# Performance work log

Measured on AMD Instinct MI355X. Metric: run time of the kernel, lower is better.

Reference implementation:

```python
import jax, jax.numpy as jnp
import numpy as np

IN_C, H1, H2, FC1, NCLS = 16, 32, 64, 128, 10
N_NODES, N_EDGES = 20000, 100000


def _glorot(key, shape):
    fan_in, fan_out = shape[0], shape[-1]
    s = jnp.sqrt(6.0 / (fan_in + fan_out))
    return jax.random.uniform(key, shape, jnp.float32, -s, s)


def setup_inputs() -> dict:
    key = jax.random.key(0)
    ks = jax.random.split(key, 20)
    x = jax.random.normal(ks[0], (N_NODES, IN_C), jnp.float32)
    edge_index = jax.random.randint(ks[1], (2, N_EDGES), 0, N_NODES, jnp.int64)
    edge_attr = jax.random.uniform(ks[2], (N_EDGES, 1), jnp.float32)
    return {
        "x": x,
        "edge_index": edge_index,
        "edge_attr": edge_attr,
        # conv1 edge-MLP: 1 -> 25 -> IN_C*H1
        "w1a": _glorot(ks[3], (1, 25)), "b1a": jnp.zeros((25,), jnp.float32),
        "w1b": _glorot(ks[4], (25, IN_C * H1)), "b1b": jnp.zeros((IN_C * H1,), jnp.float32),
        "wr1": _glorot(ks[5], (IN_C, H1)), "bias1": jnp.zeros((H1,), jnp.float32),
        # conv2 edge-MLP: 1 -> 25 -> H1*H2 (=2048)
        "w2a": _glorot(ks[6], (1, 25)), "b2a": jnp.zeros((25,), jnp.float32),
        "w2b": _glorot(ks[7], (25, H1 * H2)), "b2b": jnp.zeros((H1 * H2,), jnp.float32),
        "wr2": _glorot(ks[8], (H1, H2)), "bias2": jnp.zeros((H2,), jnp.float32),
        # trailing FCs
        "fc1_w": _glorot(ks[9], (H2, FC1)), "fc1_b": jnp.zeros((FC1,), jnp.float32),
        "fc2_w": _glorot(ks[10], (FC1, NCLS)), "fc2_b": jnp.zeros((NCLS,), jnp.float32),
    }


def _nnconv(x, src, tgt, edge_attr, wa, ba, wb, bb, wroot, bias, in_c, out_c):
    # per-edge MLP-generated weight matrix [E, in_c, out_c]
    h = jax.nn.relu(edge_attr @ wa + ba) @ wb + bb
    W = h.reshape(-1, in_c, out_c)
    # gather source feats, per-edge matmul, scatter-max to targets
    msg = jnp.einsum("ei,eio->eo", x[src], W)  # [E, out_c]
    agg = jax.ops.segment_max(msg, tgt, num_segments=x.shape[0])
    agg = jnp.where(jnp.isfinite(agg), agg, 0.0)  # nodes with no in-edges -> 0 (PyG behavior)
    return agg + x @ wroot + bias


def reference(x, edge_index, edge_attr,
              w1a, b1a, w1b, b1b, wr1, bias1,
              w2a, b2a, w2b, b2b, wr2, bias2,
              fc1_w, fc1_b, fc2_w, fc2_b):
    src, tgt = edge_index[0], edge_index[1]
    h = jax.nn.elu(_nnconv(x, src, tgt, edge_attr, w1a, b1a, w1b, b1b, wr1, bias1, IN_C, H1))
    h = jax.nn.elu(_nnconv(h, src, tgt, edge_attr, w2a, b2a, w2b, b2b, wr2, bias2, H1, H2))
    h = jax.nn.elu(h @ fc1_w + fc1_b)
    h = h @ fc2_w + fc2_b
    return jax.nn.log_softmax(h, axis=1)
```

## Files before the change

kernel.cpp:

```cpp
#include <hip/hip_runtime.h>
#include <float.h>
#include <math.h>


#define NCONST 25
#define CH1 32
#define CH2 16
#define PACK_MASK 0x1FFFF
#define TNB 4

__device__ __forceinline__ void atomicMaxFloat(float* addr, float val) {
    if (val >= 0.f) atomicMax((int*)addr, __float_as_int(val));
    else            atomicMin((unsigned int*)addr, __float_as_uint(val));
}
__device__ __forceinline__ float readlane_f(float v, int l) {
    return __int_as_float(__builtin_amdgcn_readlane(__float_as_int(v), l));
}
__device__ __forceinline__ float elu_f(float a) {
    return a > 0.f ? a : expm1f(a);
}

__global__ void fill_kernel(float* agg, int nAgg, int* ords, int nOrd, int* hist, int nH) {
    int i = blockIdx.x * blockDim.x + threadIdx.x;
    int stride = gridDim.x * blockDim.x;
    int total = nAgg + nOrd + nH;
    for (; i < total; i += stride) {
        if (i < nAgg) agg[i] = -FLT_MAX;
        else if (i < nAgg + nOrd) ords[i - nAgg] = -1;
        else hist[i - nAgg - nOrd] = 0;
    }
}

__global__ void assign_hist_kernel(const float* __restrict__ ea,
                                   const float* __restrict__ w1a, const float* __restrict__ b1a,
                                   const float* __restrict__ w2a, const float* __restrict__ b2a,
                                   int E, int* __restrict__ segpack, int* __restrict__ hist) {
    __shared__ float t1[NCONST], t2[NCONST];
    __shared__ int lh[64];
    int tid = threadIdx.x;
    if (tid < NCONST) {
        float w = w1a[tid]; t1[tid] = (w != 0.f) ? (-b1a[tid] / w) : INFINITY;
        float v = w2a[tid]; t2[tid] = (v != 0.f) ? (-b2a[tid] / v) : INFINITY;
    }
    if (tid < 64) lh[tid] = 0;
    __syncthreads();
    int e = blockIdx.x * blockDim.x + tid;
    bool valid = e < E;
    if (valid) {
        float a = ea[e];
        int j1 = 0, j2 = 0;
        for (int k = 0; k < NCONST; ++k) { j1 += (t1[k] < a); j2 += (t2[k] < a); }
        segpack[e] = j1 | (j2 << 8);
        atomicAdd(&lh[j1], 1); atomicAdd(&lh[32 + j2], 1);
    }
    __syncthreads();
    if (tid < 64 && lh[tid]) atomicAdd(&hist[tid], lh[tid]);
}

__global__ void scanpad_kernel(const int* __restrict__ hist, int* __restrict__ cur) {
    __shared__ int h[64];
    int tid = threadIdx.x;
    h[tid] = hist[tid];
    __syncthreads();
    if (tid == 0) {
        int off = 0;
        for (int j = 0; j < 26; ++j) { cur[j] = off; off += ((h[j] + CH1 - 1) / CH1) * CH1; }
    } else if (tid == 1) {
        int off = 0;
        for (int j = 0; j < 26; ++j) { cur[32 + j] = off; off += ((h[32 + j] + CH2 - 1) / CH2) * CH2; }
    }
}

__global__ void scatter_kernel(const int* __restrict__ segpack, int E, int* __restrict__ cur,
                               int* __restrict__ order1, int* __restrict__ order2) {
    __shared__ int lh[64], lb[64];
    int tid = threadIdx.x;
    if (tid < 64) lh[tid] = 0;
    __syncthreads();
    int e = blockIdx.x * blockDim.x + tid;
    bool valid = e < E;
    int j1 = 0, j2 = 0, r1 = 0, r2 = 0;
    if (valid) {
        int p = segpack[e]; j1 = p & 0xFF; j2 = p >> 8;
        r1 = atomicAdd(&lh[j1], 1); r2 = atomicAdd(&lh[32 + j2], 1);
    }
    __syncthreads();
    if (tid < 64 && lh[tid]) lb[tid] = atomicAdd(&cur[tid], lh[tid]);
    __syncthreads();
    if (valid) {
        order1[lb[j1] + r1] = (j1 << 17) | e;
        order2[lb[32 + j2] + r2] = (j2 << 17) | e;
    }
}

__global__ void build_uv_fused(const float* w1a, const float* b1a, const float* w1b, const float* b1b,
                               const float* w2a, const float* b2a, const float* w2b, const float* b2b,
                               float* U1, float* V1, float* U2, float* V2) {
    __shared__ float swa[NCONST], sba[NCONST], st[NCONST];
    __shared__ int sr[NCONST];
    __shared__ unsigned msk_sh;
    int seg = blockIdx.y;
    int bx = blockIdx.x;
    int conv = (bx < 2) ? 0 : 1;
    const float* wa = conv ? w2a : w1a;
    const float* ba = conv ? b2a : b1a;
    int tid = threadIdx.x;
    if (tid < NCONST) {
        float w = wa[tid], b = ba[tid];
        swa[tid] = w; sba[tid] = b;
        st[tid] = (w != 0.f) ? (-b / w) : INFINITY;
    }
    __syncthreads();
    if (tid < NCONST) {
        int rk = 0;
        for (int l = 0; l < NCONST; ++l) rk += (st[l] < st[tid]) ? 1 : 0;
        sr[tid] = rk;
    }
    __syncthreads();
    if (tid == 0) {
        unsigned m = 0;
        for (int k = 0; k < NCONST; ++k) {
            float w = swa[k];
            bool act = (w > 0.f) ? (seg > sr[k])
                     : (w < 0.f) ? (seg <= sr[k])
                                 : (sba[k] > 0.f);
            if (act) m |= (1u << k);
        }
        msk_sh = m;
    }
    __syncthreads();
    unsigned msk = msk_sh;
    if (conv == 0) {
        int idx = bx * 256 + tid;
        float u = 0.f, v = 0.f;
        for (int k = 0; k < NCONST; ++k)
            if (msk & (1u << k)) { float w = w1b[k * 512 + idx]; u = fmaf(swa[k], w, u); v = fmaf(sba[k], w, v); }
        v += b1b[idx];
        U1[seg * 512 + idx] = u; V1[seg * 512 + idx] = v;
    } else {
        int idx = (bx - 2) * 256 + tid;
        float u = 0.f, v = 0.f;
        for (int k = 0; k < NCONST; ++k)
            if (msk & (1u << k)) { float w = w2b[k * 2048 + idx]; u = fmaf(swa[k], w, u); v = fmaf(sba[k], w, v); }
        v += b2b[idx];
        U2[seg * 2048 + idx] = u; V2[seg * 2048 + idx] = v;
    }
}

__global__ void edge1_kernel(const float* __restrict__ xin, const int* __restrict__ src,
                             const int* __restrict__ tgt, const float* __restrict__ ea,
                             const int* __restrict__ order, int cap,
                             const float* __restrict__ U, const float* __restrict__ V,
                             float* __restrict__ agg) {
    int wid = (blockIdx.x * blockDim.x + threadIdx.x) >> 6;
    int lane = threadIdx.x & 63;
    int base = wid * CH1;
    if (base >= cap) return;
    int pk = order[base + (lane & (CH1 - 1))];
    int p0 = __builtin_amdgcn_readfirstlane(pk);
    if (p0 < 0) return;
    int seg = p0 >> 17;
    int ev = (pk < 0) ? 0 : (pk & PACK_MASK);
    int sv = src[ev], tv = tgt[ev];
    float av = ea[ev];
    int half = lane >> 5, c = lane & 31;
    float Ur[16], Vr[16];
    {
        const float* Us = U + seg * 512 + c;
        const float* Vs = V + seg * 512 + c;
#pragma unroll
        for (int i = 0; i < 16; ++i) { Ur[i] = Us[i * 32]; Vr[i] = Vs[i * 32]; }
    }
#pragma unroll
    for (int t = 0; t < CH1; t += 2) {
        int pA = __builtin_amdgcn_readlane(pk, t);
        int pB = __builtin_amdgcn_readlane(pk, t + 1);
        int sA = __builtin_amdgcn_readlane(sv, t);
        int sB = __builtin_amdgcn_readlane(sv, t + 1);
        int tA = __builtin_amdgcn_readlane(tv, t);
        int tB = __builtin_amdgcn_readlane(tv, t + 1);
        float aA = readlane_f(av, t);
        float aB = readlane_f(av, t + 1);
        const float* xA = xin + sA * 16;
        const float* xB = xin + sB * 16;
        float ah = half ? aB : aA;
        int   th = half ? tB : tA;
        int   ph = half ? pB : pA;
        float acc = 0.f;
#pragma unroll
        for (int i = 0; i < 16; ++i) {
            float xi = half ? xB[i] : xA[i];
            acc = fmaf(xi, fmaf(ah, Ur[i], Vr[i]), acc);
        }
        if (ph >= 0) atomicMaxFloat(&agg[th * 32 + c], acc);
    }
}

__global__ void edge2_kernel(const float* __restrict__ xin, const int* __restrict__ src,
                             const int* __restrict__ tgt, const float* __restrict__ ea,
                             const int* __restrict__ order, int cap,
                             const float* __restrict__ U, const float* __restrict__ V,
                             float* __restrict__ agg) {
    int wid = (blockIdx.x * blockDim.x + threadIdx.x) >> 6;
    int lane = threadIdx.x & 63;
    int base = wid * CH2;
    if (base >= cap) return;
    int pk = order[base + (lane & (CH2 - 1))];
    int p0 = __builtin_amdgcn_readfirstlane(pk);
    if (p0 < 0) return;
    int seg = p0 >> 17;
    int ev = (pk < 0) ? 0 : (pk & PACK_MASK);
    int sv = src[ev], tv = tgt[ev];
    float av = ea[ev];
    float Ur[32], Vr[32];
    {
        const float* Us = U + seg * 2048 + lane;
        const float* Vs = V + seg * 2048 + lane;
#pragma unroll
        for (int i = 0; i < 32; ++i) { Ur[i] = Us[i * 64]; Vr[i] = Vs[i * 64]; }
    }
#pragma unroll
    for (int t = 0; t < CH2; t += 2) {
        int pA = __builtin_amdgcn_readlane(pk, t);
        int pB = __builtin_amdgcn_readlane(pk, t + 1);
        int sA = __builtin_amdgcn_readlane(sv, t);
        int sB = __builtin_amdgcn_readlane(sv, t + 1);
        int tA = __builtin_amdgcn_readlane(tv, t);
        int tB = __builtin_amdgcn_readlane(tv, t + 1);
        float aA = readlane_f(av, t);
        float aB = readlane_f(av, t + 1);
        const float* xA = xin + sA * 32;
        const float* xB = xin + sB * 32;
        float accA = 0.f, accB = 0.f;
#pragma unroll
        for (int i = 0; i < 32; ++i) {
            accA = fmaf(xA[i], fmaf(aA, Ur[i], Vr[i]), accA);
            accB = fmaf(xB[i], fmaf(aB, Ur[i], Vr[i]), accB);
        }
        if (pA >= 0) atomicMaxFloat(&agg[tA * 64 + lane], accA);
        if (pB >= 0) atomicMaxFloat(&agg[tB * 64 + lane], accB);
    }
}

__global__ void node1_kernel(const float* __restrict__ xin, const float* __restrict__ agg,
                             const float* __restrict__ wroot, const float* __restrict__ bias,
                             float* __restrict__ out, int N) {
    int idx = blockIdx.x * blockDim.x + threadIdx.x;
    if (idx >= N * 32) return;
    int n = idx >> 5, c = idx & 31;
    float v = agg[idx];
    if (v == -FLT_MAX) v = 0.f;
    float acc = v + bias[c];
#pragma unroll
    for (int i = 0; i < 16; ++i) acc = fmaf(xin[n * 16 + i], wroot[i * 32 + c], acc);
    out[idx] = acc > 0.f ? acc : expm1f(acc);
}

__global__ void tail_kernel(const float* __restrict__ h1, const float* __restrict__ agg2,
                            const float* __restrict__ wr2, const float* __restrict__ bias2,
                            const float* __restrict__ fc1w, const float* __restrict__ fc1b,
                            const float* __restrict__ fc2w, const float* __restrict__ fc2b,
                            float* __restrict__ out) {
    __shared__ __align__(16) float h1sh[4][TNB][32];
    __shared__ __align__(16) float h2sh[4][TNB][64];
    __shared__ __align__(16) float h3sh[4][TNB][132];
    __shared__ __align__(16) float wTsh[10][132];
    int tid = threadIdx.x;
    int wv = tid >> 6, lane = tid & 63;

    for (int t = tid; t < 1280; t += 256) {
        int k = t / 10, j = t - k * 10;
        wTsh[j][k] = fc2w[t];
    }
    __syncthreads();

    int nb = blockIdx.x * (4 * TNB) + wv * TNB;

    {
        const float2* hp = (const float2*)(h1 + (size_t)nb * 32);
        ((float2*)&h1sh[wv][0][0])[lane] = hp[lane];
    }

    float b2v = bias2[lane];
    float ac0 = agg2[(size_t)(nb + 0) * 64 + lane];
    float ac1 = agg2[(size_t)(nb + 1) * 64 + lane];
    float ac2 = agg2[(size_t)(nb + 2) * 64 + lane];
    float ac3 = agg2[(size_t)(nb + 3) * 64 + lane];
    ac0 = (ac0 == -FLT_MAX ? 0.f : ac0) + b2v;
    ac1 = (ac1 == -FLT_MAX ? 0.f : ac1) + b2v;
    ac2 = (ac2 == -FLT_MAX ? 0.f : ac2) + b2v;
    ac3 = (ac3 == -FLT_MAX ? 0.f : ac3) + b2v;
#pragma unroll 8
    for (int i = 0; i < 32; ++i) {
        float w = wr2[i * 64 + lane];
        ac0 = fmaf(h1sh[wv][0][i], w, ac0);
        ac1 = fmaf(h1sh[wv][1][i], w, ac1);
        ac2 = fmaf(h1sh[wv][2][i], w, ac2);
        ac3 = fmaf(h1sh[wv][3][i], w, ac3);
    }
    h2sh[wv][0][lane] = elu_f(ac0);
    h2sh[wv][1][lane] = elu_f(ac1);
    h2sh[wv][2][lane] = elu_f(ac2);
    h2sh[wv][3][lane] = elu_f(ac3);

    float fb1 = fc1b[lane], fb2 = fc1b[64 + lane];
    float p0 = fb1, p1 = fb1, p2 = fb1, p3 = fb1;
    float q0 = fb2, q1 = fb2, q2 = fb2, q3 = fb2;
#pragma unroll 2
    for (int k4 = 0; k4 < 16; ++k4) {
        int k = k4 * 4;
        float wA0 = fc1w[(k + 0) * 128 + lane];
        float wB0 = fc1w[(k + 0) * 128 + 64 + lane];
        float wA1 = fc1w[(k + 1) * 128 + lane];
        float wB1 = fc1w[(k + 1) * 128 + 64 + lane];
        float wA2 = fc1w[(k + 2) * 128 + lane];
        float wB2 = fc1w[(k + 2) * 128 + 64 + lane];
        float wA3 = fc1w[(k + 3) * 128 + lane];
        float wB3 = fc1w[(k + 3) * 128 + 64 + lane];
        float4 g0 = ((const float4*)h2sh[wv][0])[k4];
        float4 g1 = ((const float4*)h2sh[wv][1])[k4];
        float4 g2 = ((const float4*)h2sh[wv][2])[k4];
        float4 g3 = ((const float4*)h2sh[wv][3])[k4];
        p0 = fmaf(g0.x, wA0, p0); p0 = fmaf(g0.y, wA1, p0);
        p0 = fmaf(g0.z, wA2, p0); p0 = fmaf(g0.w, wA3, p0);
        q0 = fmaf(g0.x, wB0, q0); q0 = fmaf(g0.y, wB1, q0);
        q0 = fmaf(g0.z, wB2, q0); q0 = fmaf(g0.w, wB3, q0);
        p1 = fmaf(g1.x, wA0, p1); p1 = fmaf(g1.y, wA1, p1);
        p1 = fmaf(g1.z, wA2, p1); p1 = fmaf(g1.w, wA3, p1);
        q1 = fmaf(g1.x, wB0, q1); q1 = fmaf(g1.y, wB1, q1);
        q1 = fmaf(g1.z, wB2, q1); q1 = fmaf(g1.w, wB3, q1);
        p2 = fmaf(g2.x, wA0, p2); p2 = fmaf(g2.y, wA1, p2);
        p2 = fmaf(g2.z, wA2, p2); p2 = fmaf(g2.w, wA3, p2);
        q2 = fmaf(g2.x, wB0, q2); q2 = fmaf(g2.y, wB1, q2);
        q2 = fmaf(g2.z, wB2, q2); q2 = fmaf(g2.w, wB3, q2);
        p3 = fmaf(g3.x, wA0, p3); p3 = fmaf(g3.y, wA1, p3);
        p3 = fmaf(g3.z, wA2, p3); p3 = fmaf(g3.w, wA3, p3);
        q3 = fmaf(g3.x, wB0, q3); q3 = fmaf(g3.y, wB1, q3);
        q3 = fmaf(g3.z, wB2, q3); q3 = fmaf(g3.w, wB3, q3);
    }
    h3sh[wv][0][lane] = elu_f(p0); h3sh[wv][0][64 + lane] = elu_f(q0);
    h3sh[wv][1][lane] = elu_f(p1); h3sh[wv][1][64 + lane] = elu_f(q1);
    h3sh[wv][2][lane] = elu_f(p2); h3sh[wv][2][64 + lane] = elu_f(q2);
    h3sh[wv][3][lane] = elu_f(p3); h3sh[wv][3][64 + lane] = elu_f(q3);

    {
        int n = lane >> 4, j = lane & 15;
        bool act = j < 10;
        int jc = act ? j : 0;
        float a = fc2b[jc];
        const float4* h3v = (const float4*)h3sh[wv][n];
        const float4* wv4 = (const float4*)wTsh[jc];
#pragma unroll
        for (int q = 0; q < 32; ++q) {
            float4 h = h3v[q];
            float4 w = wv4[q];
            a = fmaf(h.x, w.x, a);
            a = fmaf(h.y, w.y, a);
            a = fmaf(h.z, w.z, a);
            a = fmaf(h.w, w.w, a);
        }
        float lm = act ? a : -FLT_MAX;
        lm = fmaxf(lm, __shfl_xor(lm, 1, 16));
        lm = fmaxf(lm, __shfl_xor(lm, 2, 16));
        lm = fmaxf(lm, __shfl_xor(lm, 4, 16));
        lm = fmaxf(lm, __shfl_xor(lm, 8, 16));
        float ls = act ? expf(a - lm) : 0.f;
        ls += __shfl_xor(ls, 1, 16);
        ls += __shfl_xor(ls, 2, 16);
        ls += __shfl_xor(ls, 4, 16);
        ls += __shfl_xor(ls, 8, 16);
        if (act) out[(size_t)(nb + n) * 10 + j] = a - lm - logf(ls);
    }
}

extern "C" void kernel_launch(void* const* d_in, const int* in_sizes, int n_in,
                              void* d_out, int out_size, void* d_ws, size_t ws_size,
                              hipStream_t stream) {
    const float* x     = (const float*)d_in[0];
    const int*   eidx  = (const int*)d_in[1];
    const float* ea    = (const float*)d_in[2];
    const float* w1a   = (const float*)d_in[3];
    const float* b1a   = (const float*)d_in[4];
    const float* w1b   = (const float*)d_in[5];
    const float* b1b   = (const float*)d_in[6];
    const float* wr1   = (const float*)d_in[7];
    const float* bias1 = (const float*)d_in[8];
    const float* w2a   = (const float*)d_in[9];
    const float* b2a   = (const float*)d_in[10];
    const float* w2b   = (const float*)d_in[11];
    const float* b2b   = (const float*)d_in[12];
    const float* wr2   = (const float*)d_in[13];
    const float* bias2 = (const float*)d_in[14];
    const float* fc1w  = (const float*)d_in[15];
    const float* fc1b  = (const float*)d_in[16];
    const float* fc2w  = (const float*)d_in[17];
    const float* fc2b  = (const float*)d_in[18];

    const int N = in_sizes[0] / 16;
    const int E = in_sizes[2];
    const int* src = eidx;
    const int* tgt = eidx + E;

    const int cap1 = ((E + 26 * (CH1 - 1)) + CH1 - 1) / CH1 * CH1;
    const int cap2 = ((E + 26 * (CH2 - 1)) + CH2 - 1) / CH2 * CH2;

    float* ws = (float*)d_ws;
    size_t off = 0;
    int*      hist = (int*)(ws + off);      off += 64;
    int*      cur  = (int*)(ws + off);      off += 64;
    int*      segp = (int*)(ws + off);      off += E;
    int*      ord1 = (int*)(ws + off);      off += cap1;
    int*      ord2 = (int*)(ws + off);      off += cap2;
    float*    U1   = ws + off;              off += 26 * 512;
    float*    V1   = ws + off;              off += 26 * 512;
    float*    U2   = ws + off;              off += 26 * 2048;
    float*    V2   = ws + off;              off += 26 * 2048;
    float*    AGG1 = ws + off;              off += (size_t)N * 32;
    float*    AGG2 = ws + off;              off += (size_t)N * 64;
    float*    H1b  = ws + off;              off += (size_t)N * 32;

    fill_kernel<<<512, 256, 0, stream>>>(AGG1, N * 96, ord1, cap1 + cap2, hist, 64);
    assign_hist_kernel<<<(E + 255) / 256, 256, 0, stream>>>(ea, w1a, b1a, w2a, b2a, E, segp, hist);
    scanpad_kernel<<<1, 64, 0, stream>>>(hist, cur);
    scatter_kernel<<<(E + 255) / 256, 256, 0, stream>>>(segp, E, cur, ord1, ord2);
    build_uv_fused<<<dim3(10, 26), 256, 0, stream>>>(w1a, b1a, w1b, b1b, w2a, b2a, w2b, b2b,
                                                     U1, V1, U2, V2);
    {
        int waves = cap1 / CH1;
        edge1_kernel<<<(waves + 3) / 4, 256, 0, stream>>>(x, src, tgt, ea, ord1, cap1, U1, V1, AGG1);
    }
    node1_kernel<<<(N * 32 + 255) / 256, 256, 0, stream>>>(x, AGG1, wr1, bias1, H1b, N);
    {
        int waves = cap2 / CH2;
        edge2_kernel<<<(waves + 3) / 4, 256, 0, stream>>>(H1b, src, tgt, ea, ord2, cap2, U2, V2, AGG2);
    }
    tail_kernel<<<N / 16, 256, 0, stream>>>(H1b, AGG2, wr2, bias2, fc1w, fc1b, fc2w, fc2b, (float*)d_out);
}
```

Before: 198.2 us.

## Fuse whole pipeline into one cooperative persistent kernel with grid syncs

Replaces the nine separate kernel launches with one persistent cooperative kernel. The former kernels become phases separated by grid-wide barriers, and the grid is sized from occupancy up to 512 blocks. The aim is to remove per-launch overhead and inter-kernel gaps. In exchange, phases like edge processing and the tail run with far fewer blocks in grid-stride loops, and grid.sync adds its own cost. The old multi-kernel path remains as a fallback if the cooperative launch fails.

After: 703.4 us. 3.55x slower.

```diff
diff --git a/kernel.cpp b/kernel.cpp
--- a/kernel.cpp
+++ b/kernel.cpp
@@ -1,13 +1,17 @@
 #include <hip/hip_runtime.h>
+#include <hip/hip_cooperative_groups.h>
 #include <float.h>
 #include <math.h>
+
+namespace cg = cooperative_groups;
 
 
 #define NCONST 25
 #define CH1 32
 #define CH2 16
 #define PACK_MASK 0x1FFFF
-#define TNB 4
+#define NBLK_MAX 512
+#define NTHR 256
 
 __device__ __forceinline__ void atomicMaxFloat(float* addr, float val) {
     if (val >= 0.f) atomicMax((int*)addr, __float_as_int(val));
@@ -19,6 +23,366 @@
 __device__ __forceinline__ float elu_f(float a) {
     return a > 0.f ? a : expm1f(a);
 }
+
+struct MegaParams {
+    const float *x; const int *src; const int *tgt; const float *ea;
+    const float *w1a, *b1a, *w1b, *b1b, *wr1, *bias1;
+    const float *w2a, *b2a, *w2b, *b2b, *wr2, *bias2;
+    const float *fc1w, *fc1b, *fc2w, *fc2b;
+    float *out;
+    int *hist, *cur, *segp, *ord1, *ord2;
+    float *U1, *V1, *U2, *V2, *AGG1, *AGG2, *H1b;
+    int N, E, cap1, cap2;
+};
+
+__device__ __forceinline__ void gsync(cg::grid_group& grid) {
+    __threadfence();
+    grid.sync();
+    __threadfence();
+}
+
+__global__ void __launch_bounds__(NTHR) mega_kernel(MegaParams p) {
+    cg::grid_group grid = cg::this_grid();
+
+    __shared__ float t1[NCONST], t2[NCONST];
+    __shared__ int lh[64], lb[64];
+    __shared__ float swa[NCONST], sba[NCONST], stt[NCONST];
+    __shared__ int srk[NCONST];
+    __shared__ unsigned msk_sh;
+    __shared__ __align__(16) float h1sh[4][4][32];
+    __shared__ __align__(16) float h2sh[4][4][64];
+    __shared__ __align__(16) float h3sh[4][4][132];
+    __shared__ __align__(16) float wTsh[10][132];
+
+    const int tid  = threadIdx.x;
+    const int gtid = blockIdx.x * NTHR + tid;
+    const int gsz  = gridDim.x * NTHR;
+    const int lane = tid & 63;
+    const int wv   = tid >> 6;
+
+    {
+        int nAgg = p.N * 96, nOrd = p.cap1 + p.cap2;
+        int total = nAgg + nOrd + 64;
+        for (int i = gtid; i < total; i += gsz) {
+            if (i < nAgg) p.AGG1[i] = -FLT_MAX;
+            else if (i < nAgg + nOrd) p.ord1[i - nAgg] = -1;
+            else p.hist[i - nAgg - nOrd] = 0;
+        }
+        for (int v = blockIdx.x; v < 260; v += gridDim.x) {
+            int seg = v / 10;
+            int bx  = v % 10;
+            int conv = (bx < 2) ? 0 : 1;
+            const float* wa = conv ? p.w2a : p.w1a;
+            const float* ba = conv ? p.b2a : p.b1a;
+            if (tid < NCONST) {
+                float w = wa[tid], b = ba[tid];
+                swa[tid] = w; sba[tid] = b;
+                stt[tid] = (w != 0.f) ? (-b / w) : INFINITY;
+            }
+            __syncthreads();
+            if (tid < NCONST) {
+                int rk = 0;
+                for (int l = 0; l < NCONST; ++l) rk += (stt[l] < stt[tid]) ? 1 : 0;
+                srk[tid] = rk;
+            }
+            __syncthreads();
+            if (tid == 0) {
+                unsigned m = 0;
+                for (int k = 0; k < NCONST; ++k) {
+                    float w = swa[k];
+                    bool act = (w > 0.f) ? (seg > srk[k])
+                             : (w < 0.f) ? (seg <= srk[k])
+                                         : (sba[k] > 0.f);
+                    if (act) m |= (1u << k);
+                }
+                msk_sh = m;
+            }
+            __syncthreads();
+            unsigned msk = msk_sh;
+            if (conv == 0) {
+                int idx = bx * 256 + tid;
+                float u = 0.f, vv = 0.f;
+                for (int k = 0; k < NCONST; ++k)
+                    if (msk & (1u << k)) { float w = p.w1b[k * 512 + idx]; u = fmaf(swa[k], w, u); vv = fmaf(sba[k], w, vv); }
+                vv += p.b1b[idx];
+                p.U1[seg * 512 + idx] = u; p.V1[seg * 512 + idx] = vv;
+            } else {
+                int idx = (bx - 2) * 256 + tid;
+                float u = 0.f, vv = 0.f;
+                for (int k = 0; k < NCONST; ++k)
+                    if (msk & (1u << k)) { float w = p.w2b[k * 2048 + idx]; u = fmaf(swa[k], w, u); vv = fmaf(sba[k], w, vv); }
+                vv += p.b2b[idx];
+                p.U2[seg * 2048 + idx] = u; p.V2[seg * 2048 + idx] = vv;
+            }
+            __syncthreads();
+        }
+    }
+    gsync(grid);
+
+    {
+        if (tid < NCONST) {
+            float w = p.w1a[tid]; t1[tid] = (w != 0.f) ? (-p.b1a[tid] / w) : INFINITY;
+            float v2 = p.w2a[tid]; t2[tid] = (v2 != 0.f) ? (-p.b2a[tid] / v2) : INFINITY;
+        }
+        __syncthreads();
+        for (int base = blockIdx.x * NTHR; base < p.E; base += gsz) {
+            if (tid < 64) lh[tid] = 0;
+            __syncthreads();
+            int e = base + tid;
+            if (e < p.E) {
+                float a = p.ea[e];
+                int j1 = 0, j2 = 0;
+                for (int k = 0; k < NCONST; ++k) { j1 += (t1[k] < a); j2 += (t2[k] < a); }
+                p.segp[e] = j1 | (j2 << 8);
+                atomicAdd(&lh[j1], 1); atomicAdd(&lh[32 + j2], 1);
+            }
+            __syncthreads();
+            if (tid < 64 && lh[tid]) atomicAdd(&p.hist[tid], lh[tid]);
+            __syncthreads();
+        }
+    }
+    gsync(grid);
+
+    if (blockIdx.x == 0) {
+        if (tid == 0) {
+            int off = 0;
+            for (int j = 0; j < 26; ++j) { p.cur[j] = off; off += ((p.hist[j] + CH1 - 1) / CH1) * CH1; }
+        } else if (tid == 1) {
+            int off = 0;
+            for (int j = 0; j < 26; ++j) { p.cur[32 + j] = off; off += ((p.hist[32 + j] + CH2 - 1) / CH2) * CH2; }
+        }
+    }
+    gsync(grid);
+
+    {
+        for (int base = blockIdx.x * NTHR; base < p.E; base += gsz) {
+            if (tid < 64) lh[tid] = 0;
+            __syncthreads();
+            int e = base + tid;
+            bool valid = e < p.E;
+            int j1 = 0, j2 = 0, r1 = 0, r2 = 0;
+            if (valid) {
+                int pk = p.segp[e]; j1 = pk & 0xFF; j2 = pk >> 8;
+                r1 = atomicAdd(&lh[j1], 1); r2 = atomicAdd(&lh[32 + j2], 1);
+            }
+            __syncthreads();
+            if (tid < 64 && lh[tid]) lb[tid] = atomicAdd(&p.cur[tid], lh[tid]);
+            __syncthreads();
+            if (valid) {
+                p.ord1[lb[j1] + r1] = (j1 << 17) | e;
+                p.ord2[lb[32 + j2] + r2] = (j2 << 17) | e;
+            }
+            __syncthreads();
+        }
+    }
+    gsync(grid);
+
+    {
+        int gw = gtid >> 6, nw = gsz >> 6;
+        for (int w = gw; w * CH1 < p.cap1; w += nw) {
+            int base = w * CH1;
+            int pk = p.ord1[base + (lane & (CH1 - 1))];
+            int p0 = __builtin_amdgcn_readfirstlane(pk);
+            if (p0 < 0) continue;
+            int seg = p0 >> 17;
+            int ev = (pk < 0) ? 0 : (pk & PACK_MASK);
+            int sv = p.src[ev], tv = p.tgt[ev];
+            float av = p.ea[ev];
+            int half = lane >> 5, c = lane & 31;
+            float Ur[16], Vr[16];
+            {
+                const float* Us = p.U1 + seg * 512 + c;
+                const float* Vs = p.V1 + seg * 512 + c;
+#pragma unroll
+                for (int i = 0; i < 16; ++i) { Ur[i] = Us[i * 32]; Vr[i] = Vs[i * 32]; }
+            }
+#pragma unroll
+            for (int t = 0; t < CH1; t += 2) {
+                int pA = __builtin_amdgcn_readlane(pk, t);
+                int pB = __builtin_amdgcn_readlane(pk, t + 1);
+                int sA = __builtin_amdgcn_readlane(sv, t);
+                int sB = __builtin_amdgcn_readlane(sv, t + 1);
+                int tA = __builtin_amdgcn_readlane(tv, t);
+                int tB = __builtin_amdgcn_readlane(tv, t + 1);
+                float aA = readlane_f(av, t);
+                float aB = readlane_f(av, t + 1);
+                const float* xA = p.x + sA * 16;
+                const float* xB = p.x + sB * 16;
+                float ah = half ? aB : aA;
+                int   th = half ? tB : tA;
+                int   ph = half ? pB : pA;
+                float acc = 0.f;
+#pragma unroll
+                for (int i = 0; i < 16; ++i) {
+                    float xi = half ? xB[i] : xA[i];
+                    acc = fmaf(xi, fmaf(ah, Ur[i], Vr[i]), acc);
+                }
+                if (ph >= 0) atomicMaxFloat(&p.AGG1[th * 32 + c], acc);
+            }
+        }
+    }
+    gsync(grid);
+
+    {
+        for (int idx = gtid; idx < p.N * 32; idx += gsz) {
+            int n = idx >> 5, c = idx & 31;
+            float v = p.AGG1[idx];
+            if (v == -FLT_MAX) v = 0.f;
+            float acc = v + p.bias1[c];
+#pragma unroll
+            for (int i = 0; i < 16; ++i) acc = fmaf(p.x[n * 16 + i], p.wr1[i * 32 + c], acc);
+            p.H1b[idx] = acc > 0.f ? acc : expm1f(acc);
+        }
+    }
+    gsync(grid);
+
+    {
+        int gw = gtid >> 6, nw = gsz >> 6;
+        for (int w = gw; w * CH2 < p.cap2; w += nw) {
+            int base = w * CH2;
+            int pk = p.ord2[base + (lane & (CH2 - 1))];
+            int p0 = __builtin_amdgcn_readfirstlane(pk);
+            if (p0 < 0) continue;
+            int seg = p0 >> 17;
+            int ev = (pk < 0) ? 0 : (pk & PACK_MASK);
+            int sv = p.src[ev], tv = p.tgt[ev];
+            float av = p.ea[ev];
+            float Ur[32], Vr[32];
+            {
+                const float* Us = p.U2 + seg * 2048 + lane;
+                const float* Vs = p.V2 + seg * 2048 + lane;
+#pragma unroll
+                for (int i = 0; i < 32; ++i) { Ur[i] = Us[i * 64]; Vr[i] = Vs[i * 64]; }
+            }
+#pragma unroll
+            for (int t = 0; t < CH2; t += 2) {
+                int pA = __builtin_amdgcn_readlane(pk, t);
+                int pB = __builtin_amdgcn_readlane(pk, t + 1);
+                int sA = __builtin_amdgcn_readlane(sv, t);
+                int sB = __builtin_amdgcn_readlane(sv, t + 1);
+                int tA = __builtin_amdgcn_readlane(tv, t);
+                int tB = __builtin_amdgcn_readlane(tv, t + 1);
+                float aA = readlane_f(av, t);
+                float aB = readlane_f(av, t + 1);
+                const float* xA = p.H1b + sA * 32;
+                const float* xB = p.H1b + sB * 32;
+                float accA = 0.f, accB = 0.f;
+#pragma unroll
+                for (int i = 0; i < 32; ++i) {
+                    accA = fmaf(xA[i], fmaf(aA, Ur[i], Vr[i]), accA);
+                    accB = fmaf(xB[i], fmaf(aB, Ur[i], Vr[i]), accB);
+                }
+                if (pA >= 0) atomicMaxFloat(&p.AGG2[tA * 64 + lane], accA);
+                if (pB >= 0) atomicMaxFloat(&p.AGG2[tB * 64 + lane], accB);
+            }
+        }
+    }
+    gsync(grid);
+
+    {
+        for (int t = tid; t < 1280; t += NTHR) {
+            int k = t / 10, j = t - k * 10;
+            wTsh[j][k] = p.fc2w[t];
+        }
+        __syncthreads();
+        for (int g = blockIdx.x; g < p.N / 16; g += gridDim.x) {
+            int nb = g * 16 + wv * 4;
+            {
+                const float2* hp = (const float2*)(p.H1b + (size_t)nb * 32);
+                ((float2*)&h1sh[wv][0][0])[lane] = hp[lane];
+            }
+            float b2v = p.bias2[lane];
+            float ac0 = p.AGG2[(size_t)(nb + 0) * 64 + lane];
+            float ac1 = p.AGG2[(size_t)(nb + 1) * 64 + lane];
+            float ac2 = p.AGG2[(size_t)(nb + 2) * 64 + lane];
+            float ac3 = p.AGG2[(size_t)(nb + 3) * 64 + lane];
+            ac0 = (ac0 == -FLT_MAX ? 0.f : ac0) + b2v;
+            ac1 = (ac1 == -FLT_MAX ? 0.f : ac1) + b2v;
+            ac2 = (ac2 == -FLT_MAX ? 0.f : ac2) + b2v;
+            ac3 = (ac3 == -FLT_MAX ? 0.f : ac3) + b2v;
+#pragma unroll 8
+            for (int i = 0; i < 32; ++i) {
+                float w = p.wr2[i * 64 + lane];
+                ac0 = fmaf(h1sh[wv][0][i], w, ac0);
+                ac1 = fmaf(h1sh[wv][1][i], w, ac1);
+                ac2 = fmaf(h1sh[wv][2][i], w, ac2);
+                ac3 = fmaf(h1sh[wv][3][i], w, ac3);
+            }
+            h2sh[wv][0][lane] = elu_f(ac0);
+            h2sh[wv][1][lane] = elu_f(ac1);
+            h2sh[wv][2][lane] = elu_f(ac2);
+            h2sh[wv][3][lane] = elu_f(ac3);
+            float fb1 = p.fc1b[lane], fb2 = p.fc1b[64 + lane];
+            float p0 = fb1, p1 = fb1, p2 = fb1, p3 = fb1;
+            float q0 = fb2, q1 = fb2, q2 = fb2, q3 = fb2;
+#pragma unroll 2
+            for (int k4 = 0; k4 < 16; ++k4) {
+                int k = k4 * 4;
+                float wA0 = p.fc1w[(k + 0) * 128 + lane];
+                float wB0 = p.fc1w[(k + 0) * 128 + 64 + lane];
+                float wA1 = p.fc1w[(k + 1) * 128 + lane];
+                float wB1 = p.fc1w[(k + 1) * 128 + 64 + lane];
+                float wA2 = p.fc1w[(k + 2) * 128 + lane];
+                float wB2 = p.fc1w[(k + 2) * 128 + 64 + lane];
+                float wA3 = p.fc1w[(k + 3) * 128 + lane];
+                float wB3 = p.fc1w[(k + 3) * 128 + 64 + lane];
+                float4 g0 = ((const float4*)h2sh[wv][0])[k4];
+                float4 g1 = ((const float4*)h2sh[wv][1])[k4];
+                float4 g2 = ((const float4*)h2sh[wv][2])[k4];
+                float4 g3 = ((const float4*)h2sh[wv][3])[k4];
+                p0 = fmaf(g0.x, wA0, p0); p0 = fmaf(g0.y, wA1, p0);
+                p0 = fmaf(g0.z, wA2, p0); p0 = fmaf(g0.w, wA3, p0);
+                q0 = fmaf(g0.x, wB0, q0); q0 = fmaf(g0.y, wB1, q0);
+                q0 = fmaf(g0.z, wB2, q0); q0 = fmaf(g0.w, wB3, q0);
+                p1 = fmaf(g1.x, wA0, p1); p1 = fmaf(g1.y, wA1, p1);
+                p1 = fmaf(g1.z, wA2, p1); p1 = fmaf(g1.w, wA3, p1);
+                q1 = fmaf(g1.x, wB0, q1); q1 = fmaf(g1.y, wB1, q1);
+                q1 = fmaf(g1.z, wB2, q1); q1 = fmaf(g1.w, wB3, q1);
+                p2 = fmaf(g2.x, wA0, p2); p2 = fmaf(g2.y, wA1, p2);
+                p2 = fmaf(g2.z, wA2, p2); p2 = fmaf(g2.w, wA3, p2);
+                q2 = fmaf(g2.x, wB0, q2); q2 = fmaf(g2.y, wB1, q2);
+                q2 = fmaf(g2.z, wB2, q2); q2 = fmaf(g2.w, wB3, q2);
+                p3 = fmaf(g3.x, wA0, p3); p3 = fmaf(g3.y, wA1, p3);
+                p3 = fmaf(g3.z, wA2, p3); p3 = fmaf(g3.w, wA3, p3);
+                q3 = fmaf(g3.x, wB0, q3); q3 = fmaf(g3.y, wB1, q3);
+                q3 = fmaf(g3.z, wB2, q3); q3 = fmaf(g3.w, wB3, q3);
+            }
+            h3sh[wv][0][lane] = elu_f(p0); h3sh[wv][0][64 + lane] = elu_f(q0);
+            h3sh[wv][1][lane] = elu_f(p1); h3sh[wv][1][64 + lane] = elu_f(q1);
+            h3sh[wv][2][lane] = elu_f(p2); h3sh[wv][2][64 + lane] = elu_f(q2);
+            h3sh[wv][3][lane] = elu_f(p3); h3sh[wv][3][64 + lane] = elu_f(q3);
+            {
+                int n = lane >> 4, j = lane & 15;
+                bool act = j < 10;
+                int jc = act ? j : 0;
+                float a = p.fc2b[jc];
+                const float4* h3v = (const float4*)h3sh[wv][n];
+                const float4* wv4 = (const float4*)wTsh[jc];
+#pragma unroll
+                for (int q = 0; q < 32; ++q) {
+                    float4 h = h3v[q];
+                    float4 w = wv4[q];
+                    a = fmaf(h.x, w.x, a);
+                    a = fmaf(h.y, w.y, a);
+                    a = fmaf(h.z, w.z, a);
+                    a = fmaf(h.w, w.w, a);
+                }
+                float lm = act ? a : -FLT_MAX;
+                lm = fmaxf(lm, __shfl_xor(lm, 1, 16));
+                lm = fmaxf(lm, __shfl_xor(lm, 2, 16));
+                lm = fmaxf(lm, __shfl_xor(lm, 4, 16));
+                lm = fmaxf(lm, __shfl_xor(lm, 8, 16));
+                float ls = act ? expf(a - lm) : 0.f;
+                ls += __shfl_xor(ls, 1, 16);
+                ls += __shfl_xor(ls, 2, 16);
+                ls += __shfl_xor(ls, 4, 16);
+                ls += __shfl_xor(ls, 8, 16);
+                if (act) p.out[(size_t)(nb + n) * 10 + j] = a - lm - logf(ls);
+            }
+        }
+    }
+}
+
 
 __global__ void fill_kernel(float* agg, int nAgg, int* ords, int nOrd, int* hist, int nH) {
     int i = blockIdx.x * blockDim.x + threadIdx.x;
@@ -261,26 +625,22 @@
                             const float* __restrict__ fc1w, const float* __restrict__ fc1b,
                             const float* __restrict__ fc2w, const float* __restrict__ fc2b,
                             float* __restrict__ out) {
-    __shared__ __align__(16) float h1sh[4][TNB][32];
-    __shared__ __align__(16) float h2sh[4][TNB][64];
-    __shared__ __align__(16) float h3sh[4][TNB][132];
+    __shared__ __align__(16) float h1sh[4][4][32];
+    __shared__ __align__(16) float h2sh[4][4][64];
+    __shared__ __align__(16) float h3sh[4][4][132];
     __shared__ __align__(16) float wTsh[10][132];
     int tid = threadIdx.x;
     int wv = tid >> 6, lane = tid & 63;
-
     for (int t = tid; t < 1280; t += 256) {
         int k = t / 10, j = t - k * 10;
         wTsh[j][k] = fc2w[t];
     }
     __syncthreads();
-
-    int nb = blockIdx.x * (4 * TNB) + wv * TNB;
-
+    int nb = blockIdx.x * 16 + wv * 4;
     {
         const float2* hp = (const float2*)(h1 + (size_t)nb * 32);
         ((float2*)&h1sh[wv][0][0])[lane] = hp[lane];
     }
-
     float b2v = bias2[lane];
     float ac0 = agg2[(size_t)(nb + 0) * 64 + lane];
     float ac1 = agg2[(size_t)(nb + 1) * 64 + lane];
@@ -302,7 +662,6 @@
     h2sh[wv][1][lane] = elu_f(ac1);
     h2sh[wv][2][lane] = elu_f(ac2);
     h2sh[wv][3][lane] = elu_f(ac3);
-
     float fb1 = fc1b[lane], fb2 = fc1b[64 + lane];
     float p0 = fb1, p1 = fb1, p2 = fb1, p3 = fb1;
     float q0 = fb2, q1 = fb2, q2 = fb2, q3 = fb2;
@@ -342,7 +701,6 @@
     h3sh[wv][1][lane] = elu_f(p1); h3sh[wv][1][64 + lane] = elu_f(q1);
     h3sh[wv][2][lane] = elu_f(p2); h3sh[wv][2][64 + lane] = elu_f(q2);
     h3sh[wv][3][lane] = elu_f(p3); h3sh[wv][3][64 + lane] = elu_f(q3);
-
     {
         int n = lane >> 4, j = lane & 15;
         bool act = j < 10;
@@ -376,63 +734,88 @@
 extern "C" void kernel_launch(void* const* d_in, const int* in_sizes, int n_in,
                               void* d_out, int out_size, void* d_ws, size_t ws_size,
                               hipStream_t stream) {
-    const float* x     = (const float*)d_in[0];
-    const int*   eidx  = (const int*)d_in[1];
-    const float* ea    = (const float*)d_in[2];
-    const float* w1a   = (const float*)d_in[3];
-    const float* b1a   = (const float*)d_in[4];
-    const float* w1b   = (const float*)d_in[5];
-    const float* b1b   = (const float*)d_in[6];
-    const float* wr1   = (const float*)d_in[7];
-    const float* bias1 = (const float*)d_in[8];
-    const float* w2a   = (const float*)d_in[9];
-    const float* b2a   = (const float*)d_in[10];
-    const float* w2b   = (const float*)d_in[11];
-    const float* b2b   = (const float*)d_in[12];
-    const float* wr2   = (const float*)d_in[13];
-    const float* bias2 = (const float*)d_in[14];
-    const float* fc1w  = (const float*)d_in[15];
-    const float* fc1b  = (const float*)d_in[16];
-    const float* fc2w  = (const float*)d_in[17];
-    const float* fc2b  = (const float*)d_in[18];
-
-    const int N = in_sizes[0] / 16;
-    const int E = in_sizes[2];
-    const int* src = eidx;
-    const int* tgt = eidx + E;
-
-    const int cap1 = ((E + 26 * (CH1 - 1)) + CH1 - 1) / CH1 * CH1;
-    const int cap2 = ((E + 26 * (CH2 - 1)) + CH2 - 1) / CH2 * CH2;
+    MegaParams p;
+    p.x     = (const float*)d_in[0];
+    const int* eidx = (const int*)d_in[1];
+    p.ea    = (const float*)d_in[2];
+    p.w1a   = (const float*)d_in[3];
+    p.b1a   = (const float*)d_in[4];
+    p.w1b   = (const float*)d_in[5];
+    p.b1b   = (const float*)d_in[6];
+    p.wr1   = (const float*)d_in[7];
+    p.bias1 = (const float*)d_in[8];
+    p.w2a   = (const float*)d_in[9];
+    p.b2a   = (const float*)d_in[10];
+    p.w2b   = (const float*)d_in[11];
+    p.b2b   = (const float*)d_in[12];
+    p.wr2   = (const float*)d_in[13];
+    p.bias2 = (const float*)d_in[14];
+    p.fc1w  = (const float*)d_in[15];
+    p.fc1b  = (const float*)d_in[16];
+    p.fc2w  = (const float*)d_in[17];
+    p.fc2b  = (const float*)d_in[18];
+    p.out   = (float*)d_out;
+
+    p.N = in_sizes[0] / 16;
+    p.E = in_sizes[2];
+    p.src = eidx;
+    p.tgt = eidx + p.E;
+
+    p.cap1 = ((p.E + 26 * (CH1 - 1)) + CH1 - 1) / CH1 * CH1;
+    p.cap2 = ((p.E + 26 * (CH2 - 1)) + CH2 - 1) / CH2 * CH2;
 
     float* ws = (float*)d_ws;
     size_t off = 0;
-    int*      hist = (int*)(ws + off);      off += 64;
-    int*      cur  = (int*)(ws + off);      off += 64;
-    int*      segp = (int*)(ws + off);      off += E;
-    int*      ord1 = (int*)(ws + off);      off += cap1;
-    int*      ord2 = (int*)(ws + off);      off += cap2;
-    float*    U1   = ws + off;              off += 26 * 512;
-    float*    V1   = ws + off;              off += 26 * 512;
-    float*    U2   = ws + off;              off += 26 * 2048;
-    float*    V2   = ws + off;              off += 26 * 2048;
-    float*    AGG1 = ws + off;              off += (size_t)N * 32;
-    float*    AGG2 = ws + off;              off += (size_t)N * 64;
-    float*    H1b  = ws + off;              off += (size_t)N * 32;
-
-    fill_kernel<<<512, 256, 0, stream>>>(AGG1, N * 96, ord1, cap1 + cap2, hist, 64);
-    assign_hist_kernel<<<(E + 255) / 256, 256, 0, stream>>>(ea, w1a, b1a, w2a, b2a, E, segp, hist);
-    scanpad_kernel<<<1, 64, 0, stream>>>(hist, cur);
-    scatter_kernel<<<(E + 255) / 256, 256, 0, stream>>>(segp, E, cur, ord1, ord2);
-    build_uv_fused<<<dim3(10, 26), 256, 0, stream>>>(w1a, b1a, w1b, b1b, w2a, b2a, w2b, b2b,
-                                                     U1, V1, U2, V2);
-    {
-        int waves = cap1 / CH1;
-        edge1_kernel<<<(waves + 3) / 4, 256, 0, stream>>>(x, src, tgt, ea, ord1, cap1, U1, V1, AGG1);
-    }
-    node1_kernel<<<(N * 32 + 255) / 256, 256, 0, stream>>>(x, AGG1, wr1, bias1, H1b, N);
-    {
-        int waves = cap2 / CH2;
-        edge2_kernel<<<(waves + 3) / 4, 256, 0, stream>>>(H1b, src, tgt, ea, ord2, cap2, U2, V2, AGG2);
-    }
-    tail_kernel<<<N / 16, 256, 0, stream>>>(H1b, AGG2, wr2, bias2, fc1w, fc1b, fc2w, fc2b, (float*)d_out);
-}
+    p.hist = (int*)(ws + off);      off += 64;
+    p.cur  = (int*)(ws + off);      off += 64;
+    p.segp = (int*)(ws + off);      off += p.E;
+    p.ord1 = (int*)(ws + off);      off += p.cap1;
+    p.ord2 = (int*)(ws + off);      off += p.cap2;
+    p.U1   = ws + off;              off += 26 * 512;
+    p.V1   = ws + off;              off += 26 * 512;
+    p.U2   = ws + off;              off += 26 * 2048;
+    p.V2   = ws + off;              off += 26 * 2048;
+    p.AGG1 = ws + off;              off += (size_t)p.N * 32;
+    p.AGG2 = ws + off;              off += (size_t)p.N * 64;
+    p.H1b  = ws + off;              off += (size_t)p.N * 32;
+
+    static int megaGrid = -1;
+    if (megaGrid < 0) {
+        int nb = 0;
+        if (hipOccupancyMaxActiveBlocksPerMultiprocessor(&nb, mega_kernel, NTHR, 0) != hipSuccess || nb < 1)
+            nb = 1;
+        int cus = 256;
+        hipDeviceProp_t prop;
+        if (hipGetDeviceProperties(&prop, 0) == hipSuccess && prop.multiProcessorCount > 0)
+            cus = prop.multiProcessorCount;
+        long g = (long)nb * cus;
+        megaGrid = (g > NBLK_MAX) ? NBLK_MAX : (int)g;
+    }
+
+    void* args[] = { &p };
+    hipError_t err = hipLaunchCooperativeKernel((const void*)mega_kernel, dim3(megaGrid),
+                                                dim3(NTHR), args, 0, stream);
+    if (err == hipSuccess) return;
+
+    fill_kernel<<<512, 256, 0, stream>>>(p.AGG1, p.N * 96, p.ord1, p.cap1 + p.cap2, p.hist, 64);
+    assign_hist_kernel<<<(p.E + 255) / 256, 256, 0, stream>>>(p.ea, p.w1a, p.b1a, p.w2a, p.b2a,
+                                                              p.E, p.segp, p.hist);
+    scanpad_kernel<<<1, 64, 0, stream>>>(p.hist, p.cur);
+    scatter_kernel<<<(p.E + 255) / 256, 256, 0, stream>>>(p.segp, p.E, p.cur, p.ord1, p.ord2);
+    build_uv_fused<<<dim3(10, 26), 256, 0, stream>>>(p.w1a, p.b1a, p.w1b, p.b1b,
+                                                     p.w2a, p.b2a, p.w2b, p.b2b,
+                                                     p.U1, p.V1, p.U2, p.V2);
+    {
+        int waves = p.cap1 / CH1;
+        edge1_kernel<<<(waves + 3) / 4, 256, 0, stream>>>(p.x, p.src, p.tgt, p.ea, p.ord1, p.cap1,
+                                                          p.U1, p.V1, p.AGG1);
+    }
+    node1_kernel<<<(p.N * 32 + 255) / 256, 256, 0, stream>>>(p.x, p.AGG1, p.wr1, p.bias1, p.H1b, p.N);
+    {
+        int waves = p.cap2 / CH2;
+        edge2_kernel<<<(waves + 3) / 4, 256, 0, stream>>>(p.H1b, p.src, p.tgt, p.ea, p.ord2, p.cap2,
+                                                          p.U2, p.V2, p.AGG2);
+    }
+    tail_kernel<<<p.N / 16, 256, 0, stream>>>(p.H1b, p.AGG2, p.wr2, p.bias2,
+                                              p.fc1w, p.fc1b, p.fc2w, p.fc2b, p.out);
+}
```
